# Performance work log

Hardware: AMD Instinct MI355X
Metric: run time of the kernel (lower is better)

The kernel has to match this reference:

```python
import jax, jax.numpy as jnp
import numpy as np

ALPHA = 0.01  # LeakyReLU negative slope

def _leaky(x):
    return jnp.where(x > 0, x, ALPHA * x)

def _conv(x, w, b):
    # x: NHWC, w: HWIO, valid padding, stride 1
    return jax.lax.conv_general_dilated(x, w, (1, 1), 'VALID',
        dimension_numbers=('NHWC', 'HWIO', 'NHWC')) + b

def _maxpool2(x):
    return jax.lax.reduce_window(x, -jnp.inf, jax.lax.max,
        (1, 2, 2, 1), (1, 2, 2, 1), 'VALID')

def setup_inputs() -> dict:
    key = jax.random.key(0)
    ks = jax.random.split(key, 32)
    B, S, H = 32, 197, 256
    FLAT = 47 * 62 * 64  # after conv/pool trunk = 186496
    def w(k, shape, fan_in):
        return jax.random.normal(k, shape, dtype=jnp.float32) * np.float32(1.0 / np.sqrt(fan_in))
    inp = {
        'x': jax.random.normal(ks[0], (B, S, H), dtype=jnp.float32),
        'conv1_w': w(ks[1], (3, 3, 1, 32), 9), 'conv1_b': jnp.zeros((32,), jnp.float32),
        'conv2_w': w(ks[2], (3, 3, 32, 64), 288), 'conv2_b': jnp.zeros((64,), jnp.float32),
        'w_c1': w(ks[3], (FLAT, 512), FLAT), 'b_c1': jnp.zeros((512,), jnp.float32),
        'w_c2': w(ks[4], (512, 256), 512), 'b_c2': jnp.zeros((256,), jnp.float32),
        'w_co': w(ks[5], (256, 225 * 13), 256), 'b_co': jnp.zeros((225 * 13,), jnp.float32),
        'w_sm': w(ks[6], (13, 13), 13), 'b_sm': jnp.zeros((13,), jnp.float32),
        'w_r1': w(ks[7], (FLAT, 256), FLAT), 'b_r1': jnp.zeros((256,), jnp.float32),
        'w_r2': w(ks[8], (256, 128), 256), 'b_r2': jnp.zeros((128,), jnp.float32),
        'w_r3': w(ks[9], (128, 128), 128), 'b_r3': jnp.zeros((128,), jnp.float32),
        'w_r4': w(ks[10], (128, 64), 128), 'b_r4': jnp.zeros((64,), jnp.float32),
        'w_ro': w(ks[11], (64, 225 * 4), 64), 'b_ro': jnp.zeros((225 * 4,), jnp.float32),
        'w_sg': w(ks[12], (4, 4), 4), 'b_sg': jnp.zeros((4,), jnp.float32),
    }
    return inp

def reference(x, conv1_w, conv1_b, conv2_w, conv2_b,
              w_c1, b_c1, w_c2, b_c2, w_co, b_co, w_sm, b_sm,
              w_r1, b_r1, w_r2, b_r2, w_r3, b_r3, w_r4, b_r4,
              w_ro, b_ro, w_sg, b_sg):
    # CNN trunk on expanded hidden state (B, S, H, 1)
    h = x[..., None]
    h = jax.nn.relu(_conv(h, conv1_w, conv1_b))
    h = _maxpool2(h)
    h = jax.nn.relu(_conv(h, conv2_w, conv2_b))
    h = _maxpool2(h)
    h = h.reshape(h.shape[0], -1)  # (B, 186496)
    # classification branch (dropout is identity at inference)
    y = _leaky(h @ w_c1 + b_c1)
    y = _leaky(y @ w_c2 + b_c2)
    y = _leaky(y @ w_co + b_co).reshape(-1, 225, 13)
    # 225-step loop of shared Dense(13, softmax) heads -> one batched matmul
    class_out = jax.nn.softmax(jnp.einsum('bpi,ij->bpj', y, w_sm) + b_sm, axis=-1)
    z = _leaky(h @ w_r1 + b_r1)
    z = _leaky(z @ w_r2 + b_r2)
    z = _leaky(z @ w_r3 + b_r3)
    z = _leaky(z @ w_r4 + b_r4)
    z = (z @ w_ro + b_ro).reshape(-1, 225, 4)
    reg_out = jax.nn.sigmoid(jnp.einsum('bpi,ij->bpj', z, w_sg) + b_sg)
    return class_out, reg_out
```

## Files before the change

kernel.cpp:

```cpp
#include <hip/hip_runtime.h>
#include <hip/hip_bf16.h>

#define ALPHA 0.01f

typedef __attribute__((ext_vector_type(8))) __bf16 bf16x8;
typedef __attribute__((ext_vector_type(4))) float f32x4;

#define BATCH 32
#define P1H 97
#define P1W 127
#define P2W 62
#define FLAT 186496
#define GK 512
#define NGK 365
#define PSTRIDE1 16448
#define PSTRIDE2 8256

static __device__ __forceinline__ unsigned short f2bf(float x) {
  union { float f; unsigned u; } c; c.f = x;
  unsigned r = c.u + 0x7fffu + ((c.u >> 16) & 1u);
  return (unsigned short)(r >> 16);
}

static __device__ __forceinline__ unsigned pack2bf(float lo, float hi) {
  union { float f; unsigned u; } a, b;
  a.f = lo; b.f = hi;
  unsigned ra = (a.u + 0x7fffu + ((a.u >> 16) & 1u)) >> 16;
  unsigned rb = (b.u + 0x7fffu + ((b.u >> 16) & 1u)) & 0xffff0000u;
  return ra | rb;
}

__global__ __launch_bounds__(256) void conv1_pool(const float* __restrict__ x,
    const float* __restrict__ w1, const float* __restrict__ b1,
    unsigned short* __restrict__ p1) {
  int pid = blockIdx.x * 256 + threadIdx.x;
  if (pid >= BATCH * P1H * P1W) return;
  int b = pid / (P1H * P1W);
  int rem = pid - b * (P1H * P1W);
  int ph = rem / P1W;
  int pw = rem - ph * P1W;
  const float* xb = x + ((b * 197 + 2 * ph) * 256 + 2 * pw);
  float in[4][4];
#pragma unroll
  for (int r = 0; r < 4; ++r) {
    float2 v0 = *reinterpret_cast<const float2*>(xb + r * 256);
    float2 v1 = *reinterpret_cast<const float2*>(xb + r * 256 + 2);
    in[r][0] = v0.x; in[r][1] = v0.y; in[r][2] = v1.x; in[r][3] = v1.y;
  }
  unsigned pk[16];
#pragma unroll
  for (int c = 0; c < 32; ++c) {
    float s00 = b1[c], s01 = s00, s10 = s00, s11 = s00;
#pragma unroll
    for (int ky = 0; ky < 3; ++ky)
#pragma unroll
      for (int kx = 0; kx < 3; ++kx) {
        float w = w1[(ky * 3 + kx) * 32 + c];
        s00 = fmaf(in[ky][kx], w, s00);
        s01 = fmaf(in[ky][kx + 1], w, s01);
        s10 = fmaf(in[ky + 1][kx], w, s10);
        s11 = fmaf(in[ky + 1][kx + 1], w, s11);
      }
    float m = fmaxf(fmaxf(s00, s01), fmaxf(s10, s11));
    m = fmaxf(m, 0.0f);
    unsigned short u = f2bf(m);
    if (c & 1) pk[c >> 1] |= ((unsigned)u) << 16;
    else pk[c >> 1] = (unsigned)u;
  }
  uint4* dst = reinterpret_cast<uint4*>(p1 + (size_t)pid * 32);
#pragma unroll
  for (int g = 0; g < 4; ++g)
    dst[g] = make_uint4(pk[g * 4], pk[g * 4 + 1], pk[g * 4 + 2], pk[g * 4 + 3]);
}

__global__ __launch_bounds__(256) void repack_w2(const float* __restrict__ w2,
                                                 unsigned short* __restrict__ bpack) {
  int o = blockIdx.x * 256 + threadIdx.x;
  if (o >= 9 * 4 * 512) return;
  int f = o >> 9;
  int within = o & 511;
  int lane = within >> 3, j = within & 7;
  int tap = f >> 2, nf = f & 3;
  int k = ((lane >> 4) << 3) + j;
  int n = nf * 16 + (lane & 15);
  bpack[o] = f2bf(w2[(tap * 32 + k) * 64 + n]);
}

__global__ __launch_bounds__(256) void conv2_pool(const unsigned short* __restrict__ p1,
    const unsigned short* __restrict__ bpack, const float* __restrict__ b2,
    unsigned short* __restrict__ hbf) {
  __shared__ alignas(16) unsigned char lds_buf[65536];
  int prow = blockIdx.x, b = blockIdx.y;
  int tid = threadIdx.x;
  int lane = tid & 63, wid = tid >> 6;
  {
    const uint4* src = reinterpret_cast<const uint4*>(bpack);
    uint4* dst = reinterpret_cast<uint4*>(lds_buf);
    for (int i = tid; i < 2304; i += 256) dst[i] = src[i];
  }
  __syncthreads();
  int row = lane & 15, kg = lane >> 4;
  int rowbase[4];
  int coff[4][3];
#pragma unroll
  for (int mf = 0; mf < 4; ++mf) {
    int m = wid * 64 + mf * 16 + row;
    int cro = m >> 7, cc = m & 127;
    rowbase[mf] = ((b * 97 + 2 * prow + cro) * 127) * 32 + kg * 8;
#pragma unroll
    for (int kx = 0; kx < 3; ++kx) {
      int ic = cc + kx; if (ic > 126) ic = 126;
      coff[mf][kx] = ic * 32;
    }
  }
  f32x4 acc[4][4];
#pragma unroll
  for (int i = 0; i < 4; ++i)
#pragma unroll
    for (int j = 0; j < 4; ++j) acc[i][j] = (f32x4){0.f, 0.f, 0.f, 0.f};

  const bf16x8* bl = reinterpret_cast<const bf16x8*>(lds_buf);
#pragma unroll
  for (int ky = 0; ky < 3; ++ky) {
#pragma unroll
    for (int kx = 0; kx < 3; ++kx) {
      int tap = ky * 3 + kx;
      bf16x8 a[4];
#pragma unroll
      for (int mf = 0; mf < 4; ++mf) {
        int addr = rowbase[mf] + ky * (127 * 32) + coff[mf][kx];
        a[mf] = *reinterpret_cast<const bf16x8*>(p1 + addr);
      }
      bf16x8 bf[4];
#pragma unroll
      for (int nf = 0; nf < 4; ++nf) bf[nf] = bl[(tap * 4 + nf) * 64 + lane];
#pragma unroll
      for (int nf = 0; nf < 4; ++nf)
#pragma unroll
        for (int mf = 0; mf < 4; ++mf)
          acc[mf][nf] = __builtin_amdgcn_mfma_f32_16x16x32_bf16(a[mf], bf[nf], acc[mf][nf], 0, 0, 0);
    }
  }
  __syncthreads();
  float* stage = reinterpret_cast<float*>(lds_buf);
#pragma unroll
  for (int mf = 0; mf < 4; ++mf)
#pragma unroll
    for (int nf = 0; nf < 4; ++nf) {
      int ch = nf * 16 + (lane & 15);
      float bias = b2[ch];
#pragma unroll
      for (int j = 0; j < 4; ++j) {
        int m = wid * 64 + mf * 16 + (lane >> 4) * 4 + j;
        float v = acc[mf][nf][j] + bias;
        stage[m * 64 + ch] = fmaxf(v, 0.f);
      }
    }
  __syncthreads();
  unsigned short* hb = hbf + (size_t)b * FLAT + prow * (P2W * 64);
  for (int o = tid; o < P2W * 64; o += 256) {
    int pw = o >> 6, ch = o & 63;
    int c0 = 2 * pw;
    float v = fmaxf(fmaxf(stage[c0 * 64 + ch], stage[(c0 + 1) * 64 + ch]),
                    fmaxf(stage[(128 + c0) * 64 + ch], stage[(129 + c0) * 64 + ch]));
    hb[o] = f2bf(v);
  }
}

__global__ __launch_bounds__(512) void gemm_mfma(
    const float* __restrict__ w_c1, const float* __restrict__ w_r1,
    const unsigned short* __restrict__ hbf,
    float* __restrict__ part1, float* __restrict__ part2) {
  int kc = blockIdx.x, tile = blockIdx.y;
  int t = threadIdx.x, lane = t & 63, wid = t >> 6;
  int k0 = kc * GK;
  int klen = FLAT - k0; if (klen > GK) klen = GK;
  int nsteps = klen >> 5;
  const float* W; int N, n0;
  if (tile < 2) { W = w_c1; N = 512; n0 = tile * 256; }
  else          { W = w_r1; N = 256; n0 = 0; }
  int cl = lane & 15, kg = lane >> 4;
  const float* Wb0 = W + (size_t)(k0 + kg * 8) * N + (n0 + wid * 32 + cl);
  const float* Wb1 = Wb0 + 16;
  const unsigned short* ha = hbf + (size_t)cl * FLAT + k0 + kg * 8;

  f32x4 acc[2][2];
#pragma unroll
  for (int i = 0; i < 2; ++i)
#pragma unroll
    for (int j = 0; j < 2; ++j) acc[i][j] = (f32x4){0.f, 0.f, 0.f, 0.f};

  float e0[8], e1[8];
  union U4 { unsigned u[4]; bf16x8 v; };
  U4 b0, b1;

#pragma unroll
  for (int j = 0; j < 8; ++j) {
    e0[j] = Wb0[(size_t)j * N];
    e1[j] = Wb1[(size_t)j * N];
  }
#pragma unroll
  for (int p = 0; p < 4; ++p) {
    b0.u[p] = pack2bf(e0[2 * p], e0[2 * p + 1]);
    b1.u[p] = pack2bf(e1[2 * p], e1[2 * p + 1]);
  }

  for (int kt = 0; kt < nsteps; ++kt) {
    if (kt + 1 < nsteps) {
      const float* wp0 = Wb0 + (size_t)(kt + 1) * 32 * N;
      const float* wp1 = Wb1 + (size_t)(kt + 1) * 32 * N;
#pragma unroll
      for (int j = 0; j < 8; ++j) {
        e0[j] = wp0[(size_t)j * N];
        e1[j] = wp1[(size_t)j * N];
      }
    }
    bf16x8 a0 = *reinterpret_cast<const bf16x8*>(ha + kt * 32);
    bf16x8 a1 = *reinterpret_cast<const bf16x8*>(ha + (size_t)16 * FLAT + kt * 32);
    acc[0][0] = __builtin_amdgcn_mfma_f32_16x16x32_bf16(a0, b0.v, acc[0][0], 0, 0, 0);
    acc[1][0] = __builtin_amdgcn_mfma_f32_16x16x32_bf16(a1, b0.v, acc[1][0], 0, 0, 0);
    acc[0][1] = __builtin_amdgcn_mfma_f32_16x16x32_bf16(a0, b1.v, acc[0][1], 0, 0, 0);
    acc[1][1] = __builtin_amdgcn_mfma_f32_16x16x32_bf16(a1, b1.v, acc[1][1], 0, 0, 0);
    if (kt + 1 < nsteps) {
#pragma unroll
      for (int p = 0; p < 4; ++p) {
        b0.u[p] = pack2bf(e0[2 * p], e0[2 * p + 1]);
        b1.u[p] = pack2bf(e1[2 * p], e1[2 * p + 1]);
      }
    }
  }

  if (tile < 2) {
    float* out = part1 + (size_t)kc * PSTRIDE1;
#pragma unroll
    for (int mf = 0; mf < 2; ++mf)
#pragma unroll
      for (int nf = 0; nf < 2; ++nf)
#pragma unroll
        for (int j = 0; j < 4; ++j) {
          int m = mf * 16 + kg * 4 + j;
          int n = n0 + wid * 32 + nf * 16 + cl;
          out[m * 512 + n] = acc[mf][nf][j];
        }
  } else {
    float* out = part2 + (size_t)kc * PSTRIDE2;
#pragma unroll
    for (int mf = 0; mf < 2; ++mf)
#pragma unroll
      for (int nf = 0; nf < 2; ++nf)
#pragma unroll
        for (int j = 0; j < 4; ++j) {
          int m = mf * 16 + kg * 4 + j;
          int n = wid * 32 + nf * 16 + cl;
          out[m * 256 + n] = acc[mf][nf][j];
        }
  }
}

__global__ __launch_bounds__(256) void reduce_big(const float* __restrict__ part1,
    const float* __restrict__ part2, const float* __restrict__ b_c1,
    const float* __restrict__ b_r1, float* __restrict__ y1, float* __restrict__ z1) {
  __shared__ float red[8][32];
  int b = blockIdx.x, t = threadIdx.x;
  int oo = t & 31, j = t >> 5;
  float s = 0.f;
  if (b < 512) {
    const float* p = part1 + b * 32 + oo;
    for (int c = j; c < NGK; c += 8) s += p[(size_t)c * PSTRIDE1];
    red[j][oo] = s;
    __syncthreads();
    if (t < 32) {
      float r = 0.f;
#pragma unroll
      for (int jj = 0; jj < 8; ++jj) r += red[jj][t];
      int o = b * 32 + t;
      r += b_c1[o & 511];
      y1[o] = r > 0.f ? r : ALPHA * r;
    }
  } else {
    const float* p = part2 + (b - 512) * 32 + oo;
    for (int c = j; c < NGK; c += 8) s += p[(size_t)c * PSTRIDE2];
    red[j][oo] = s;
    __syncthreads();
    if (t < 32) {
      float r = 0.f;
#pragma unroll
      for (int jj = 0; jj < 8; ++jj) r += red[jj][t];
      int u = (b - 512) * 32 + t;
      r += b_r1[u & 255];
      z1[u] = r > 0.f ? r : ALPHA * r;
    }
  }
}

__global__ __launch_bounds__(256) void tail_all(
    const float* __restrict__ y1g, const float* __restrict__ z1g,
    const float* __restrict__ w_c2, const float* __restrict__ b_c2,
    const float* __restrict__ w_co, const float* __restrict__ b_co,
    const float* __restrict__ w_sm, const float* __restrict__ b_sm,
    const float* __restrict__ w_r2, const float* __restrict__ b_r2,
    const float* __restrict__ w_r3, const float* __restrict__ b_r3,
    const float* __restrict__ w_r4, const float* __restrict__ b_r4,
    const float* __restrict__ w_ro, const float* __restrict__ b_ro,
    const float* __restrict__ w_sg, const float* __restrict__ b_sg,
    float* __restrict__ class_out, float* __restrict__ reg_out) {
  int tile = blockIdx.x, m = blockIdx.y, t = threadIdx.x;
  if (tile < 8) {
    __shared__ float ly1[512], ly2[256], ly3[29 * 13];
    ly1[t] = y1g[m * 512 + t];
    ly1[t + 256] = y1g[m * 512 + 256 + t];
    __syncthreads();
    {
      float s = b_c2[t];
      for (int k = 0; k < 512; ++k) s = fmaf(ly1[k], w_c2[k * 256 + t], s);
      ly2[t] = s > 0.f ? s : ALPHA * s;
    }
    __syncthreads();
    int p0 = tile * 29;
    int np = 225 - p0; if (np > 29) np = 29;
    int ncols = np * 13;
    for (int n = t; n < ncols; n += 256) {
      int col = p0 * 13 + n;
      float s = b_co[col];
      for (int k = 0; k < 256; ++k) s = fmaf(ly2[k], w_co[k * 2925 + col], s);
      ly3[n] = s > 0.f ? s : ALPHA * s;
    }
    __syncthreads();
    if (t < np) {
      float v[13], l[13], mx = -1e30f;
#pragma unroll
      for (int i = 0; i < 13; ++i) v[i] = ly3[t * 13 + i];
#pragma unroll
      for (int j = 0; j < 13; ++j) {
        float s = b_sm[j];
#pragma unroll
        for (int i = 0; i < 13; ++i) s = fmaf(v[i], w_sm[i * 13 + j], s);
        l[j] = s; mx = fmaxf(mx, s);
      }
      float sum = 0.f;
#pragma unroll
      for (int j = 0; j < 13; ++j) { l[j] = expf(l[j] - mx); sum += l[j]; }
      float inv = 1.f / sum;
      float* o = class_out + ((size_t)m * 225 + p0 + t) * 13;
#pragma unroll
      for (int j = 0; j < 13; ++j) o[j] = l[j] * inv;
    }
  } else {
    __shared__ float lz1[256], lz2[128], lz3[128], lz4[64], lzo[57 * 4];
    lz1[t] = z1g[m * 256 + t];
    __syncthreads();
    if (t < 128) {
      float s = b_r2[t];
      for (int k = 0; k < 256; ++k) s = fmaf(lz1[k], w_r2[k * 128 + t], s);
      lz2[t] = s > 0.f ? s : ALPHA * s;
    }
    __syncthreads();
    if (t < 128) {
      float s = b_r3[t];
      for (int k = 0; k < 128; ++k) s = fmaf(lz2[k], w_r3[k * 128 + t], s);
      lz3[t] = s > 0.f ? s : ALPHA * s;
    }
    __syncthreads();
    if (t < 64) {
      float s = b_r4[t];
      for (int k = 0; k < 128; ++k) s = fmaf(lz3[k], w_r4[k * 64 + t], s);
      lz4[t] = s > 0.f ? s : ALPHA * s;
    }
    __syncthreads();
    int p0 = (tile - 8) * 57;
    int np = 225 - p0; if (np > 57) np = 57;
    int ncols = np * 4;
    for (int n = t; n < ncols; n += 256) {
      int col = p0 * 4 + n;
      float s = b_ro[col];
#pragma unroll
      for (int k = 0; k < 64; ++k) s = fmaf(lz4[k], w_ro[k * 900 + col], s);
      lzo[n] = s;
    }
    __syncthreads();
    if (t < np) {
      float z[4];
#pragma unroll
      for (int i = 0; i < 4; ++i) z[i] = lzo[t * 4 + i];
      float* ro = reg_out + ((size_t)m * 225 + p0 + t) * 4;
#pragma unroll
      for (int j = 0; j < 4; ++j) {
        float s = b_sg[j];
#pragma unroll
        for (int i = 0; i < 4; ++i) s = fmaf(z[i], w_sg[i * 4 + j], s);
        ro[j] = 1.f / (1.f + expf(-s));
      }
    }
  }
}

#define OFF_P1     ((size_t)0)
#define OFF_BPACK  ((size_t)25229312)
#define OFF_H      ((size_t)25266176)
#define OFF_PART1  ((size_t)37201920)
#define OFF_PART2  ((size_t)61216000)
#define OFF_Y1     ((size_t)73269760)
#define OFF_Z1     ((size_t)73335296)

extern "C" void kernel_launch(void* const* d_in, const int* in_sizes, int n_in,
                              void* d_out, int out_size, void* d_ws, size_t ws_size,
                              hipStream_t stream) {
  const float* x     = (const float*)d_in[0];
  const float* w1    = (const float*)d_in[1];
  const float* b1    = (const float*)d_in[2];
  const float* w2    = (const float*)d_in[3];
  const float* b2    = (const float*)d_in[4];
  const float* w_c1  = (const float*)d_in[5];
  const float* b_c1  = (const float*)d_in[6];
  const float* w_c2  = (const float*)d_in[7];
  const float* b_c2  = (const float*)d_in[8];
  const float* w_co  = (const float*)d_in[9];
  const float* b_co  = (const float*)d_in[10];
  const float* w_sm  = (const float*)d_in[11];
  const float* b_sm  = (const float*)d_in[12];
  const float* w_r1  = (const float*)d_in[13];
  const float* b_r1  = (const float*)d_in[14];
  const float* w_r2  = (const float*)d_in[15];
  const float* b_r2  = (const float*)d_in[16];
  const float* w_r3  = (const float*)d_in[17];
  const float* b_r3  = (const float*)d_in[18];
  const float* w_r4  = (const float*)d_in[19];
  const float* b_r4  = (const float*)d_in[20];
  const float* w_ro  = (const float*)d_in[21];
  const float* b_ro  = (const float*)d_in[22];
  const float* w_sg  = (const float*)d_in[23];
  const float* b_sg  = (const float*)d_in[24];

  char* ws = (char*)d_ws;
  unsigned short* p1    = (unsigned short*)(ws + OFF_P1);
  unsigned short* bpack = (unsigned short*)(ws + OFF_BPACK);
  unsigned short* hbf   = (unsigned short*)(ws + OFF_H);
  float*          part1 = (float*)(ws + OFF_PART1);
  float*          part2 = (float*)(ws + OFF_PART2);
  float*          y1    = (float*)(ws + OFF_Y1);
  float*          z1    = (float*)(ws + OFF_Z1);

  float* class_out = (float*)d_out;
  float* reg_out   = (float*)d_out + 32 * 225 * 13;

  conv1_pool<<<1540, 256, 0, stream>>>(x, w1, b1, p1);
  repack_w2<<<72, 256, 0, stream>>>(w2, bpack);
  conv2_pool<<<dim3(47, 32), 256, 0, stream>>>(p1, bpack, b2, hbf);
  gemm_mfma<<<dim3(NGK, 3), 512, 0, stream>>>(w_c1, w_r1, hbf, part1, part2);
  reduce_big<<<768, 256, 0, stream>>>(part1, part2, b_c1, b_r1, y1, z1);
  tail_all<<<dim3(12, 32), 256, 0, stream>>>(y1, z1,
      w_c2, b_c2, w_co, b_co, w_sm, b_sm,
      w_r2, b_r2, w_r3, b_r3, w_r4, b_r4,
      w_ro, b_ro, w_sg, b_sg, class_out, reg_out);
}
```

Measured before the change: 280.8 us.

## Split big GEMM into templated per-weight launches with smaller blocks and A prefetch

The fused split-K GEMM over w_c1 and w_r1 is split into two template instantiations with compile-time N and output stride. Blocks shrink from 512 to 256 threads, each covering 128 columns, with launch_bounds asking for 6 blocks per CU to raise occupancy. The activation loads (A fragments) are now double-buffered one k-step ahead, like the weights already were. This costs an extra kernel launch and more registers for the prefetched A fragments.

```diff
diff --git a/kernel.cpp b/kernel.cpp
--- a/kernel.cpp
+++ b/kernel.cpp
@@ -167,22 +167,20 @@
   }
 }
 
-__global__ __launch_bounds__(512) void gemm_mfma(
-    const float* __restrict__ w_c1, const float* __restrict__ w_r1,
-    const unsigned short* __restrict__ hbf,
-    float* __restrict__ part1, float* __restrict__ part2) {
-  int kc = blockIdx.x, tile = blockIdx.y;
+template <int N, int CSTRIDE>
+__global__ __launch_bounds__(256, 6) void gemm_mfma(const float* __restrict__ W,
+    const unsigned short* __restrict__ hbf, float* __restrict__ part) {
+  int kc = blockIdx.x;
+  int n0 = blockIdx.y * 128;
   int t = threadIdx.x, lane = t & 63, wid = t >> 6;
   int k0 = kc * GK;
   int klen = FLAT - k0; if (klen > GK) klen = GK;
   int nsteps = klen >> 5;
-  const float* W; int N, n0;
-  if (tile < 2) { W = w_c1; N = 512; n0 = tile * 256; }
-  else          { W = w_r1; N = 256; n0 = 0; }
   int cl = lane & 15, kg = lane >> 4;
   const float* Wb0 = W + (size_t)(k0 + kg * 8) * N + (n0 + wid * 32 + cl);
   const float* Wb1 = Wb0 + 16;
-  const unsigned short* ha = hbf + (size_t)cl * FLAT + k0 + kg * 8;
+  const unsigned short* ha0 = hbf + (size_t)cl * FLAT + k0 + kg * 8;
+  const unsigned short* ha1 = ha0 + (size_t)16 * FLAT;
 
   f32x4 acc[2][2];
 #pragma unroll
@@ -193,7 +191,10 @@
   float e0[8], e1[8];
   union U4 { unsigned u[4]; bf16x8 v; };
   U4 b0, b1;
-
+  bf16x8 a0, a1, a0n, a1n;
+
+  a0 = *reinterpret_cast<const bf16x8*>(ha0);
+  a1 = *reinterpret_cast<const bf16x8*>(ha1);
 #pragma unroll
   for (int j = 0; j < 8; ++j) {
     e0[j] = Wb0[(size_t)j * N];
@@ -206,7 +207,10 @@
   }
 
   for (int kt = 0; kt < nsteps; ++kt) {
-    if (kt + 1 < nsteps) {
+    bool pf = (kt + 1 < nsteps);
+    if (pf) {
+      a0n = *reinterpret_cast<const bf16x8*>(ha0 + (kt + 1) * 32);
+      a1n = *reinterpret_cast<const bf16x8*>(ha1 + (kt + 1) * 32);
       const float* wp0 = Wb0 + (size_t)(kt + 1) * 32 * N;
       const float* wp1 = Wb1 + (size_t)(kt + 1) * 32 * N;
 #pragma unroll
@@ -215,46 +219,31 @@
         e1[j] = wp1[(size_t)j * N];
       }
     }
-    bf16x8 a0 = *reinterpret_cast<const bf16x8*>(ha + kt * 32);
-    bf16x8 a1 = *reinterpret_cast<const bf16x8*>(ha + (size_t)16 * FLAT + kt * 32);
     acc[0][0] = __builtin_amdgcn_mfma_f32_16x16x32_bf16(a0, b0.v, acc[0][0], 0, 0, 0);
     acc[1][0] = __builtin_amdgcn_mfma_f32_16x16x32_bf16(a1, b0.v, acc[1][0], 0, 0, 0);
     acc[0][1] = __builtin_amdgcn_mfma_f32_16x16x32_bf16(a0, b1.v, acc[0][1], 0, 0, 0);
     acc[1][1] = __builtin_amdgcn_mfma_f32_16x16x32_bf16(a1, b1.v, acc[1][1], 0, 0, 0);
-    if (kt + 1 < nsteps) {
+    if (pf) {
 #pragma unroll
       for (int p = 0; p < 4; ++p) {
         b0.u[p] = pack2bf(e0[2 * p], e0[2 * p + 1]);
         b1.u[p] = pack2bf(e1[2 * p], e1[2 * p + 1]);
       }
-    }
-  }
-
-  if (tile < 2) {
-    float* out = part1 + (size_t)kc * PSTRIDE1;
-#pragma unroll
-    for (int mf = 0; mf < 2; ++mf)
-#pragma unroll
-      for (int nf = 0; nf < 2; ++nf)
-#pragma unroll
-        for (int j = 0; j < 4; ++j) {
-          int m = mf * 16 + kg * 4 + j;
-          int n = n0 + wid * 32 + nf * 16 + cl;
-          out[m * 512 + n] = acc[mf][nf][j];
-        }
-  } else {
-    float* out = part2 + (size_t)kc * PSTRIDE2;
-#pragma unroll
-    for (int mf = 0; mf < 2; ++mf)
-#pragma unroll
-      for (int nf = 0; nf < 2; ++nf)
-#pragma unroll
-        for (int j = 0; j < 4; ++j) {
-          int m = mf * 16 + kg * 4 + j;
-          int n = wid * 32 + nf * 16 + cl;
-          out[m * 256 + n] = acc[mf][nf][j];
-        }
-  }
+      a0 = a0n; a1 = a1n;
+    }
+  }
+
+  float* out = part + (size_t)kc * CSTRIDE;
+#pragma unroll
+  for (int mf = 0; mf < 2; ++mf)
+#pragma unroll
+    for (int nf = 0; nf < 2; ++nf)
+#pragma unroll
+      for (int j = 0; j < 4; ++j) {
+        int m = mf * 16 + kg * 4 + j;
+        int n = n0 + wid * 32 + nf * 16 + cl;
+        out[m * N + n] = acc[mf][nf][j];
+      }
 }
 
 __global__ __launch_bounds__(256) void reduce_big(const float* __restrict__ part1,
@@ -446,7 +435,8 @@
   conv1_pool<<<1540, 256, 0, stream>>>(x, w1, b1, p1);
   repack_w2<<<72, 256, 0, stream>>>(w2, bpack);
   conv2_pool<<<dim3(47, 32), 256, 0, stream>>>(p1, bpack, b2, hbf);
-  gemm_mfma<<<dim3(NGK, 3), 512, 0, stream>>>(w_c1, w_r1, hbf, part1, part2);
+  gemm_mfma<512, PSTRIDE1><<<dim3(NGK, 4), 256, 0, stream>>>(w_c1, hbf, part1);
+  gemm_mfma<256, PSTRIDE2><<<dim3(NGK, 2), 256, 0, stream>>>(w_r1, hbf, part2);
   reduce_big<<<768, 256, 0, stream>>>(part1, part2, b_c1, b_r1, y1, z1);
   tail_all<<<dim3(12, 32), 256, 0, stream>>>(y1, z1,
       w_c2, b_c2, w_co, b_co, w_sm, b_sm,
```

New measurement: 275.8 us. Within noise of the previous version (-1.8%).
